# Kernel tuning notes

Measured on AMD Instinct MI355X. Metric: run time of the kernel, lower is better.

Reference implementation:

```python
import jax, jax.numpy as jnp
import numpy as np

N = 16384          # num nodes
E = 262144         # num edges (before self loops)
IN_DIM = 128
HID = 128
OUT = 2
TRIM = 0.1
MAX_DEG = 48       # padded max in-degree (incl. self loop); safe bound for Poisson(16)+1
BN_EPS = 1e-5


def _lin_params(key, fan_in, fan_out):
    kw, kb = jax.random.split(key)
    s = 1.0 / np.sqrt(fan_in)
    W = jax.random.uniform(kw, (fan_in, fan_out), jnp.float32, -s, s)
    b = jax.random.uniform(kb, (fan_out,), jnp.float32, -s, s)
    return W, b


def setup_inputs() -> dict:
    key = jax.random.key(0)
    ks = jax.random.split(key, 8)
    x = jax.random.normal(ks[0], (N, IN_DIM), jnp.float32)
    edge_index = jax.random.randint(ks[1], (2, E), 0, N, jnp.int32)
    Wl0, bl0 = _lin_params(ks[2], IN_DIM, HID)
    Wr0, br0 = _lin_params(ks[3], IN_DIM, HID)
    Wl1, bl1 = _lin_params(ks[4], HID, HID)
    Wr1, br1 = _lin_params(ks[5], HID, HID)
    Wl2, bl2 = _lin_params(ks[6], HID, OUT)
    Wr2, br2 = _lin_params(ks[7], HID, OUT)
    g0 = jnp.ones((HID,), jnp.float32); be0 = jnp.zeros((HID,), jnp.float32)
    g1 = jnp.ones((HID,), jnp.float32); be1 = jnp.zeros((HID,), jnp.float32)
    return dict(x=x, edge_index=edge_index,
                Wl0=Wl0, bl0=bl0, Wr0=Wr0, br0=br0, g0=g0, be0=be0,
                Wl1=Wl1, bl1=bl1, Wr1=Wr1, br1=br1, g1=g1, be1=be1,
                Wl2=Wl2, bl2=bl2, Wr2=Wr2, br2=br2)


def _forward(edge_index, x, Wl0, bl0, Wr0, br0, g0, be0,
             Wl1, bl1, Wr1, br1, g1, be1, Wl2, bl2, Wr2, br2):
    loops = jnp.arange(N, dtype=edge_index.dtype)
    row = jnp.concatenate([edge_index[0], loops])   # source nodes
    col = jnp.concatenate([edge_index[1], loops])   # destination nodes
    counts = jax.ops.segment_sum(jnp.ones_like(col), col, num_segments=N)  # in-degree, int
    deg = jnp.maximum(counts, 1).astype(x.dtype)
    norm = 1.0 / deg[col]                            # 1/deg(dst), per edge

    # Edge ordering grouped by destination node; rank = slot within the node's group.
    perm = jnp.argsort(col, stable=True)
    col_s = col[perm]
    starts = jnp.cumsum(counts) - counts
    rank = jnp.arange(col.shape[0], dtype=counts.dtype) - starts[col_s]
    node_id = jnp.where(rank < MAX_DEG, col_s, N)    # overflow slots -> OOB, dropped by scatter

    t = jnp.maximum(1, jnp.floor(counts.astype(jnp.float32) * TRIM).astype(counts.dtype))
    tcnt = counts - 2 * t
    pos = jnp.arange(MAX_DEG)[None, :]
    sel = (pos >= t[:, None]) & (pos < (counts - t)[:, None])   # [N, MAX_DEG]
    use_trim = (counts >= 5) & (tcnt > 0)
    inv_tcnt = 1.0 / jnp.maximum(tcnt, 1).astype(x.dtype)

    def trimmed_scatter(msg):
        # plain mean fallback
        mean = jax.ops.segment_sum(msg, col, num_segments=N) / deg[:, None]
        d = msg.shape[1]
        # padded per-node buffer; +inf pads sort to the end (never selected by `sel`)
        dense = jnp.full((N, MAX_DEG, d), jnp.inf, msg.dtype)
        dense = dense.at[node_id, rank].set(msg[perm], mode='drop')
        sdense = jnp.sort(dense, axis=1)             # per-feature sort within each node
        tmean = jnp.sum(jnp.where(sel[:, :, None], sdense, 0.0), axis=1) * inv_tcnt[:, None]
        return jnp.where(use_trim[:, None], tmean, mean)

    def conv(h, Wl, bl, Wr, br):
        msg = (h @ Wl + bl)[row] * norm[:, None]
        return trimmed_scatter(msg) + h @ Wr + br

    bn_scale = jnp.float32(1.0 / np.sqrt(1.0 + BN_EPS))  # eval-mode BN: running mean 0, var 1
    h = conv(x, Wl0, bl0, Wr0, br0)
    h = jax.nn.relu(h * bn_scale * g0 + be0)
    h = conv(h, Wl1, bl1, Wr1, br1)
    h = jax.nn.relu(h * bn_scale * g1 + be1)
    return conv(h, Wl2, bl2, Wr2, br2)


def reference(x, edge_index, Wl0, bl0, Wr0, br0, g0, be0,
              Wl1, bl1, Wr1, br1, g1, be1, Wl2, bl2, Wr2, br2):
    return _forward(edge_index, x, Wl0, bl0, Wr0, br0, g0, be0,
                    Wl1, bl1, Wr1, br1, g1, be1, Wl2, bl2, Wr2, br2)
```

## Files before the change

kernel.cpp:

```cpp
#include <hip/hip_runtime.h>
#include <hip/hip_bf16.h>
#include <hip/hip_fp16.h>
#include <math.h>

#define GN    16384
#define MAXD  48
#define BN_SCALE 0.9999950000374998f

typedef __attribute__((ext_vector_type(8))) short short8;
typedef __attribute__((ext_vector_type(4))) float f32x4;
typedef _Float16 __attribute__((ext_vector_type(2))) h2v;

__device__ inline short f2bf(float x) {
    unsigned u = __float_as_uint(x);
    return (short)((u + 0x7fffu + ((u >> 16) & 1u)) >> 16);
}
__device__ inline float bf2f(short s) {
    return __uint_as_float(((unsigned)(unsigned short)s) << 16);
}

__global__ __launch_bounds__(256) void k_build(
    const int* __restrict__ src, const int* __restrict__ dst, int E,
    int* __restrict__ adj, int* __restrict__ fill,
    const float* __restrict__ Wl0, const float* __restrict__ Wr0,
    const float* __restrict__ Wl1, const float* __restrict__ Wr1,
    short* __restrict__ W5)
{
    int idx = blockIdx.x * 256 + threadIdx.x;
    if (idx < E) {
        int dv = dst[idx];
        int slot = atomicAdd(&fill[dv], 1);
        if (slot < MAXD) adj[dv * MAXD + slot] = src[idx];
        return;
    }
    idx -= E;
    if (idx < GN) {
        int slot = atomicAdd(&fill[idx], 1);
        if (slot < MAXD) adj[idx * MAXD + slot] = idx;
        return;
    }
    idx -= GN;
    if (idx >= 2 * 8192) return;
    int layer = idx >> 13;
    int g     = idx & 8191;
    int split = (g >> 12) & 1;
    int ks    = (g >> 10) & 3;
    int nt    = (g >> 6) & 15;
    int l     = g & 63;
    int q = l >> 4, r = l & 15;
    int n = nt * 16 + r;
    const float* W = (n < 128) ? (layer ? Wl1 : Wl0) : (layer ? Wr1 : Wr0);
    int ncol = n & 127;
    short8 out;
    #pragma unroll
    for (int j = 0; j < 8; ++j) {
        int k = ks * 32 + (j >> 2) * 16 + q * 4 + (j & 3);
        float wv = W[k * 128 + ncol];
        short hi = f2bf(wv);
        out[j] = split ? f2bf(wv - bf2f(hi)) : hi;
    }
    *reinterpret_cast<short8*>(W5 + ((size_t)layer * 8192 + g) * 8) = out;
}

__global__ __launch_bounds__(256, 2) void k_gemm(
    const float* __restrict__ X, const short* __restrict__ W5,
    const float* __restrict__ bl, const float* __restrict__ br,
    _Float16* __restrict__ HL, float* __restrict__ HR)
{
    const int tid = threadIdx.x;
    const int w = tid >> 6, l = tid & 63;
    const int q = l >> 4, r = l & 15;
    const int half = w & 1, nhalf = w >> 1;
    const int rowA = blockIdx.x * 32 + half * 16 + r;

    short8 Ahi[4], Alo[4];
    const float4* xp = reinterpret_cast<const float4*>(X + (size_t)rowA * 128);
    #pragma unroll
    for (int h = 0; h < 8; ++h) {
        float4 v = xp[h * 4 + q];
        float xv[4] = {v.x, v.y, v.z, v.w};
        int ks = h >> 1, hk = h & 1;
        #pragma unroll
        for (int j = 0; j < 4; ++j) {
            short hi = f2bf(xv[j]);
            Ahi[ks][hk * 4 + j] = hi;
            Alo[ks][hk * 4 + j] = f2bf(xv[j] - bf2f(hi));
        }
    }

    const float* bias = nhalf ? br : bl;
    f32x4 acc[8];
    #pragma unroll
    for (int nt = 0; nt < 8; ++nt) {
        float b = bias[nt * 16 + r];
        acc[nt] = (f32x4){b, b, b, b};
    }

    #pragma unroll
    for (int ks = 0; ks < 4; ++ks) {
        #pragma unroll
        for (int nt = 0; nt < 8; ++nt) {
            int ntg = nhalf * 8 + nt;
            short8 Bhi = *reinterpret_cast<const short8*>(
                W5 + ((size_t)((ks) * 16 + ntg) * 64 + l) * 8);
            short8 Blo = *reinterpret_cast<const short8*>(
                W5 + ((size_t)((4 + ks) * 16 + ntg) * 64 + l) * 8);
            acc[nt] = __builtin_amdgcn_mfma_f32_16x16x32_bf16(Ahi[ks], Bhi, acc[nt], 0, 0, 0);
            acc[nt] = __builtin_amdgcn_mfma_f32_16x16x32_bf16(Ahi[ks], Blo, acc[nt], 0, 0, 0);
            acc[nt] = __builtin_amdgcn_mfma_f32_16x16x32_bf16(Alo[ks], Bhi, acc[nt], 0, 0, 0);
        }
    }

    const int rb = blockIdx.x * 32 + half * 16 + 4 * q;
    if (nhalf == 0) {
        #pragma unroll
        for (int nt = 0; nt < 8; ++nt) {
            int c = nt * 16 + r;
            #pragma unroll
            for (int j = 0; j < 4; ++j)
                HL[(size_t)(rb + j) * 128 + c] = (_Float16)acc[nt][j];
        }
    } else {
        #pragma unroll
        for (int nt = 0; nt < 8; ++nt) {
            int c = nt * 16 + r;
            #pragma unroll
            for (int j = 0; j < 4; ++j)
                HR[(size_t)(rb + j) * 128 + c] = acc[nt][j];
        }
    }
}

struct F2 { float x, y; };
__device__ inline F2 f2min(F2 a, F2 b) { return {fminf(a.x, b.x), fminf(a.y, b.y)}; }
__device__ inline F2 f2max(F2 a, F2 b) { return {fmaxf(a.x, b.x), fmaxf(a.y, b.y)}; }

__global__ __launch_bounds__(256) void k_agg(
    const _Float16* __restrict__ HL, const float* __restrict__ HR,
    const int* __restrict__ adj, const int* __restrict__ fill,
    const float* __restrict__ g, const float* __restrict__ be,
    float* __restrict__ hb)
{
    __shared__ int sadj[4][MAXD];
    const int tid = threadIdx.x, w = tid >> 6, l = tid & 63;
    const int v = blockIdx.x * 4 + w;
    const int cnt = fill[v];
    const int d = min(cnt, MAXD);
    if (l < d) sadj[w][l] = adj[v * MAXD + l] * 128;
    __syncthreads();

    const int f2i = l * 2;
    F2 tot = {0.f, 0.f};
    F2 s0 = { INFINITY,  INFINITY}, s1 = s0, s2 = s0, s3 = s0;
    F2 l0 = {-INFINITY, -INFINITY}, l1 = l0, l2 = l0, l3 = l0;

    if (cnt < 20) {
        for (int i = 0; i < d; ++i) {
            h2v hv = *reinterpret_cast<const h2v*>(HL + sadj[w][i] + f2i);
            F2 x = {(float)hv[0], (float)hv[1]};
            tot.x += x.x; tot.y += x.y;
            s0 = f2min(s0, x);
            l0 = f2max(l0, x);
        }
    } else {
        for (int i = 0; i < d; ++i) {
            h2v hv = *reinterpret_cast<const h2v*>(HL + sadj[w][i] + f2i);
            F2 x = {(float)hv[0], (float)hv[1]};
            tot.x += x.x; tot.y += x.y;
            F2 a = x;
            F2 t0 = f2min(s0, a); a = f2max(s0, a); s0 = t0;
            F2 t1 = f2min(s1, a); a = f2max(s1, a); s1 = t1;
            F2 t2 = f2min(s2, a); a = f2max(s2, a); s2 = t2;
            s3 = f2min(s3, a);
            F2 b = x;
            F2 u0 = f2max(l0, b); b = f2min(l0, b); l0 = u0;
            F2 u1 = f2max(l1, b); b = f2min(l1, b); l1 = u1;
            F2 u2 = f2max(l2, b); b = f2min(l2, b); l2 = u2;
            l3 = f2max(l3, b);
        }
    }

    int t = (int)floorf((float)cnt * 0.1f);
    if (t < 1) t = 1;
    int tcnt = cnt - 2 * t;
    bool use_trim = (cnt >= 5) && (tcnt > 0);
    float dd = (float)cnt;
    F2 res;
    if (use_trim) {
        int tt = min(t, 4);
        F2 bot = s0, top = l0;
        if (tt > 1) { bot.x += s1.x; bot.y += s1.y; top.x += l1.x; top.y += l1.y; }
        if (tt > 2) { bot.x += s2.x; bot.y += s2.y; top.x += l2.x; top.y += l2.y; }
        if (tt > 3) { bot.x += s3.x; bot.y += s3.y; top.x += l3.x; top.y += l3.y; }
        float inv = 1.0f / (dd * (float)tcnt);
        res.x = (tot.x - bot.x - top.x) * inv;
        res.y = (tot.y - bot.y - top.y) * inv;
    } else {
        float inv = 1.0f / (dd * dd);
        res.x = tot.x * inv;
        res.y = tot.y * inv;
    }

    const float2 hrv = *reinterpret_cast<const float2*>(HR + (size_t)v * 128 + f2i);
    float v0 = fmaxf((res.x + hrv.x) * (BN_SCALE * g[f2i])     + be[f2i],     0.f);
    float v1 = fmaxf((res.y + hrv.y) * (BN_SCALE * g[f2i + 1]) + be[f2i + 1], 0.f);
    float2 o = {v0, v1};
    *reinterpret_cast<float2*>(hb + (size_t)v * 128 + f2i) = o;
}

__global__ __launch_bounds__(256) void k_gemm_out(
    const float* __restrict__ H,
    const float* __restrict__ Wl, const float* __restrict__ bl,
    const float* __restrict__ Wr, const float* __restrict__ br,
    float* __restrict__ hl2, float* __restrict__ hr2)
{
    int idx = blockIdx.x * 256 + threadIdx.x;
    int v = idx >> 1, j = idx & 1;
    const float4* h = reinterpret_cast<const float4*>(H + (size_t)v * 128);
    float a = 0.f, rr = 0.f;
    #pragma unroll
    for (int k4 = 0; k4 < 32; ++k4) {
        float4 hv = h[k4];
        float xs[4] = {hv.x, hv.y, hv.z, hv.w};
        #pragma unroll
        for (int c = 0; c < 4; ++c) {
            int k = 4 * k4 + c;
            a  = fmaf(xs[c], Wl[k * 2 + j], a);
            rr = fmaf(xs[c], Wr[k * 2 + j], rr);
        }
    }
    hl2[idx] = a + bl[j];
    hr2[idx] = rr + br[j];
}

__global__ __launch_bounds__(256) void k_agg_out(
    const float* __restrict__ hl2, const float* __restrict__ hr2,
    const int* __restrict__ adj, const int* __restrict__ fill,
    float* __restrict__ out)
{
    int idx = blockIdx.x * 256 + threadIdx.x;
    int v = idx >> 1, j = idx & 1;
    int cnt = fill[v];
    int d = min(cnt, MAXD);
    const int* ap = adj + v * MAXD;

    float total = 0.f;
    float s0 = INFINITY, s1 = INFINITY, s2 = INFINITY, s3 = INFINITY;
    float l0 = -INFINITY, l1 = -INFINITY, l2 = -INFINITY, l3 = -INFINITY;
    for (int i = 0; i < d; ++i) {
        float x = hl2[ap[i] * 2 + j];
        total += x;
        float a = x;
        float t0 = fminf(s0, a); a = fmaxf(s0, a); s0 = t0;
        float t1 = fminf(s1, a); a = fmaxf(s1, a); s1 = t1;
        float t2 = fminf(s2, a); a = fmaxf(s2, a); s2 = t2;
        s3 = fminf(s3, a);
        float b = x;
        float u0 = fmaxf(l0, b); b = fminf(l0, b); l0 = u0;
        float u1 = fmaxf(l1, b); b = fminf(l1, b); l1 = u1;
        float u2 = fmaxf(l2, b); b = fminf(l2, b); l2 = u2;
        l3 = fmaxf(l3, b);
    }

    int t = (int)floorf((float)cnt * 0.1f);
    if (t < 1) t = 1;
    int tcnt = cnt - 2 * t;
    bool use_trim = (cnt >= 5) && (tcnt > 0);
    float dd = (float)cnt;
    float res;
    if (use_trim) {
        int tt = min(t, 4);
        float bot = s0, top = l0;
        if (tt > 1) { bot += s1; top += l1; }
        if (tt > 2) { bot += s2; top += l2; }
        if (tt > 3) { bot += s3; top += l3; }
        res = (total - bot - top) / (dd * (float)tcnt);
    } else {
        res = total / (dd * dd);
    }
    out[idx] = res + hr2[idx];
}

extern "C" void kernel_launch(void* const* d_in, const int* in_sizes, int n_in,
                              void* d_out, int out_size, void* d_ws, size_t ws_size,
                              hipStream_t stream)
{
    const float* x   = (const float*)d_in[0];
    const int*   ei  = (const int*)d_in[1];
    const int    E   = in_sizes[1] / 2;
    const float* Wl0 = (const float*)d_in[2];
    const float* bl0 = (const float*)d_in[3];
    const float* Wr0 = (const float*)d_in[4];
    const float* br0 = (const float*)d_in[5];
    const float* g0  = (const float*)d_in[6];
    const float* be0 = (const float*)d_in[7];
    const float* Wl1 = (const float*)d_in[8];
    const float* bl1 = (const float*)d_in[9];
    const float* Wr1 = (const float*)d_in[10];
    const float* br1 = (const float*)d_in[11];
    const float* g1  = (const float*)d_in[12];
    const float* be1 = (const float*)d_in[13];
    const float* Wl2 = (const float*)d_in[14];
    const float* bl2 = (const float*)d_in[15];
    const float* Wr2 = (const float*)d_in[16];
    const float* br2 = (const float*)d_in[17];
    float* out = (float*)d_out;

    char* w = (char*)d_ws;
    int*      adj  = (int*)w;       w += (size_t)GN * MAXD * 4;
    int*      fill = (int*)w;       w += (size_t)GN * 4;
    _Float16* HL   = (_Float16*)w;  w += (size_t)GN * 128 * 2;
    float*    HR   = (float*)w;     w += (size_t)GN * 128 * 4;
    float*    hb   = (float*)w;     w += (size_t)GN * 128 * 4;
    short*    W5   = (short*)w;     w += (size_t)2 * 8192 * 16;
    float*    hl2  = (float*)w;     w += (size_t)GN * 2 * 4;
    float*    hr2  = (float*)w;     w += (size_t)GN * 2 * 4;

    hipMemsetAsync(fill, 0, (size_t)GN * 4, stream);
    {
        int total = E + GN + 2 * 8192;
        k_build<<<(total + 255) / 256, 256, 0, stream>>>(
            ei, ei + E, E, adj, fill, Wl0, Wr0, Wl1, Wr1, W5);
    }

    k_gemm<<<GN / 32, 256, 0, stream>>>(x, W5, bl0, br0, HL, HR);
    k_agg <<<GN / 4, 256, 0, stream>>>(HL, HR, adj, fill, g0, be0, hb);
    k_gemm<<<GN / 32, 256, 0, stream>>>(hb, W5 + (size_t)8192 * 8, bl1, br1, HL, HR);
    k_agg <<<GN / 4, 256, 0, stream>>>(HL, HR, adj, fill, g1, be1, hb);
    k_gemm_out<<<GN * 2 / 256, 256, 0, stream>>>(hb, Wl2, bl2, Wr2, br2, hl2, hr2);
    k_agg_out <<<GN * 2 / 256, 256, 0, stream>>>(hl2, hr2, adj, fill, out);
}
```

Before: 200.2 us.

## Fuse all GNN stages into one cooperative persistent megakernel with grid syncs

Replaces the memset plus six separate kernel launches with a single cooperative kernel that runs each stage as a grid-stride phase separated by grid.sync(). The memset is folded in by having each node's fill counter start at 1 with its self loop in slot 0. Edge insertion into the adjacency lists now shares a phase with the first GEMM, so the two overlap. This removes launch gaps and inter-kernel drains, but the grid is capped at 512 blocks of 256 threads (2 per CU), which limits occupancy in the gather-heavy aggregation phases and adds grid-wide barrier cost.

```diff
diff --git a/kernel.cpp b/kernel.cpp
--- a/kernel.cpp
+++ b/kernel.cpp
@@ -1,7 +1,9 @@
 #include <hip/hip_runtime.h>
-#include <hip/hip_bf16.h>
+#include <hip/hip_cooperative_groups.h>
 #include <hip/hip_fp16.h>
 #include <math.h>
+
+namespace cg = cooperative_groups;
 
 #define GN    16384
 #define MAXD  48
@@ -19,114 +21,83 @@
     return __uint_as_float(((unsigned)(unsigned short)s) << 16);
 }
 
-__global__ __launch_bounds__(256) void k_build(
-    const int* __restrict__ src, const int* __restrict__ dst, int E,
-    int* __restrict__ adj, int* __restrict__ fill,
-    const float* __restrict__ Wl0, const float* __restrict__ Wr0,
-    const float* __restrict__ Wl1, const float* __restrict__ Wr1,
-    short* __restrict__ W5)
-{
-    int idx = blockIdx.x * 256 + threadIdx.x;
-    if (idx < E) {
-        int dv = dst[idx];
-        int slot = atomicAdd(&fill[dv], 1);
-        if (slot < MAXD) adj[dv * MAXD + slot] = src[idx];
-        return;
-    }
-    idx -= E;
-    if (idx < GN) {
-        int slot = atomicAdd(&fill[idx], 1);
-        if (slot < MAXD) adj[idx * MAXD + slot] = idx;
-        return;
-    }
-    idx -= GN;
-    if (idx >= 2 * 8192) return;
-    int layer = idx >> 13;
-    int g     = idx & 8191;
-    int split = (g >> 12) & 1;
-    int ks    = (g >> 10) & 3;
-    int nt    = (g >> 6) & 15;
-    int l     = g & 63;
-    int q = l >> 4, r = l & 15;
-    int n = nt * 16 + r;
-    const float* W = (n < 128) ? (layer ? Wl1 : Wl0) : (layer ? Wr1 : Wr0);
-    int ncol = n & 127;
-    short8 out;
-    #pragma unroll
-    for (int j = 0; j < 8; ++j) {
-        int k = ks * 32 + (j >> 2) * 16 + q * 4 + (j & 3);
-        float wv = W[k * 128 + ncol];
-        short hi = f2bf(wv);
-        out[j] = split ? f2bf(wv - bf2f(hi)) : hi;
-    }
-    *reinterpret_cast<short8*>(W5 + ((size_t)layer * 8192 + g) * 8) = out;
-}
-
-__global__ __launch_bounds__(256, 2) void k_gemm(
-    const float* __restrict__ X, const short* __restrict__ W5,
-    const float* __restrict__ bl, const float* __restrict__ br,
-    _Float16* __restrict__ HL, float* __restrict__ HR)
+struct Params {
+    const float* x; const int* ei; int E;
+    const float *Wl0, *bl0, *Wr0, *br0, *g0, *be0;
+    const float *Wl1, *bl1, *Wr1, *br1, *g1, *be1;
+    const float *Wl2, *bl2, *Wr2, *br2;
+    float* out;
+    int* adj; int* fill;
+    _Float16* HL; float* HR; float* hb;
+    short* W5; float* hl2; float* hr2;
+};
+
+__device__ inline void gemm_phase(const float* __restrict__ X,
+                                  const short* __restrict__ W5,
+                                  const float* __restrict__ bl,
+                                  const float* __restrict__ br,
+                                  _Float16* __restrict__ HL,
+                                  float* __restrict__ HR)
 {
     const int tid = threadIdx.x;
     const int w = tid >> 6, l = tid & 63;
     const int q = l >> 4, r = l & 15;
     const int half = w & 1, nhalf = w >> 1;
-    const int rowA = blockIdx.x * 32 + half * 16 + r;
-
-    short8 Ahi[4], Alo[4];
-    const float4* xp = reinterpret_cast<const float4*>(X + (size_t)rowA * 128);
-    #pragma unroll
-    for (int h = 0; h < 8; ++h) {
-        float4 v = xp[h * 4 + q];
-        float xv[4] = {v.x, v.y, v.z, v.w};
-        int ks = h >> 1, hk = h & 1;
-        #pragma unroll
-        for (int j = 0; j < 4; ++j) {
-            short hi = f2bf(xv[j]);
-            Ahi[ks][hk * 4 + j] = hi;
-            Alo[ks][hk * 4 + j] = f2bf(xv[j] - bf2f(hi));
-        }
-    }
-
-    const float* bias = nhalf ? br : bl;
-    f32x4 acc[8];
-    #pragma unroll
-    for (int nt = 0; nt < 8; ++nt) {
-        float b = bias[nt * 16 + r];
-        acc[nt] = (f32x4){b, b, b, b};
-    }
-
-    #pragma unroll
-    for (int ks = 0; ks < 4; ++ks) {
+
+    for (int tile = blockIdx.x; tile < GN / 32; tile += gridDim.x) {
+        const int rowA = tile * 32 + half * 16 + r;
+        short8 Ahi[4], Alo[4];
+        const float4* xp = reinterpret_cast<const float4*>(X + (size_t)rowA * 128);
+        #pragma unroll
+        for (int h = 0; h < 8; ++h) {
+            float4 v = xp[h * 4 + q];
+            float xv[4] = {v.x, v.y, v.z, v.w};
+            int ks = h >> 1, hk = h & 1;
+            #pragma unroll
+            for (int j = 0; j < 4; ++j) {
+                short hi = f2bf(xv[j]);
+                Ahi[ks][hk * 4 + j] = hi;
+                Alo[ks][hk * 4 + j] = f2bf(xv[j] - bf2f(hi));
+            }
+        }
+        const float* bias = nhalf ? br : bl;
+        f32x4 acc[8];
         #pragma unroll
         for (int nt = 0; nt < 8; ++nt) {
-            int ntg = nhalf * 8 + nt;
-            short8 Bhi = *reinterpret_cast<const short8*>(
-                W5 + ((size_t)((ks) * 16 + ntg) * 64 + l) * 8);
-            short8 Blo = *reinterpret_cast<const short8*>(
-                W5 + ((size_t)((4 + ks) * 16 + ntg) * 64 + l) * 8);
-            acc[nt] = __builtin_amdgcn_mfma_f32_16x16x32_bf16(Ahi[ks], Bhi, acc[nt], 0, 0, 0);
-            acc[nt] = __builtin_amdgcn_mfma_f32_16x16x32_bf16(Ahi[ks], Blo, acc[nt], 0, 0, 0);
-            acc[nt] = __builtin_amdgcn_mfma_f32_16x16x32_bf16(Alo[ks], Bhi, acc[nt], 0, 0, 0);
-        }
-    }
-
-    const int rb = blockIdx.x * 32 + half * 16 + 4 * q;
-    if (nhalf == 0) {
-        #pragma unroll
-        for (int nt = 0; nt < 8; ++nt) {
-            int c = nt * 16 + r;
-            #pragma unroll
-            for (int j = 0; j < 4; ++j)
-                HL[(size_t)(rb + j) * 128 + c] = (_Float16)acc[nt][j];
-        }
-    } else {
-        #pragma unroll
-        for (int nt = 0; nt < 8; ++nt) {
-            int c = nt * 16 + r;
-            #pragma unroll
-            for (int j = 0; j < 4; ++j)
-                HR[(size_t)(rb + j) * 128 + c] = acc[nt][j];
+            float b = bias[nt * 16 + r];
+            acc[nt] = (f32x4){b, b, b, b};
+        }
+        #pragma unroll
+        for (int ks = 0; ks < 4; ++ks) {
+            #pragma unroll
+            for (int nt = 0; nt < 8; ++nt) {
+                int ntg = nhalf * 8 + nt;
+                short8 Bhi = *reinterpret_cast<const short8*>(
+                    W5 + ((size_t)(ks * 16 + ntg) * 64 + l) * 8);
+                short8 Blo = *reinterpret_cast<const short8*>(
+                    W5 + ((size_t)((4 + ks) * 16 + ntg) * 64 + l) * 8);
+                acc[nt] = __builtin_amdgcn_mfma_f32_16x16x32_bf16(Ahi[ks], Bhi, acc[nt], 0, 0, 0);
+                acc[nt] = __builtin_amdgcn_mfma_f32_16x16x32_bf16(Ahi[ks], Blo, acc[nt], 0, 0, 0);
+                acc[nt] = __builtin_amdgcn_mfma_f32_16x16x32_bf16(Alo[ks], Bhi, acc[nt], 0, 0, 0);
+            }
+        }
+        const int rb = tile * 32 + half * 16 + 4 * q;
+        if (nhalf == 0) {
+            #pragma unroll
+            for (int nt = 0; nt < 8; ++nt) {
+                int c = nt * 16 + r;
+                #pragma unroll
+                for (int j = 0; j < 4; ++j)
+                    HL[(size_t)(rb + j) * 128 + c] = (_Float16)acc[nt][j];
+            }
+        } else {
+            #pragma unroll
+            for (int nt = 0; nt < 8; ++nt) {
+                int c = nt * 16 + r;
+                #pragma unroll
+                for (int j = 0; j < 4; ++j)
+                    HR[(size_t)(rb + j) * 128 + c] = acc[nt][j];
+            }
         }
     }
 }
@@ -135,198 +106,238 @@
 __device__ inline F2 f2min(F2 a, F2 b) { return {fminf(a.x, b.x), fminf(a.y, b.y)}; }
 __device__ inline F2 f2max(F2 a, F2 b) { return {fmaxf(a.x, b.x), fmaxf(a.y, b.y)}; }
 
-__global__ __launch_bounds__(256) void k_agg(
-    const _Float16* __restrict__ HL, const float* __restrict__ HR,
-    const int* __restrict__ adj, const int* __restrict__ fill,
-    const float* __restrict__ g, const float* __restrict__ be,
-    float* __restrict__ hb)
+__device__ inline void agg_phase(const _Float16* __restrict__ HL,
+                                 const float* __restrict__ HR,
+                                 const int* __restrict__ adj,
+                                 const int* __restrict__ fill,
+                                 const float* __restrict__ g,
+                                 const float* __restrict__ be,
+                                 float* __restrict__ hb,
+                                 int sadj[4][MAXD])
 {
+    const int tid = threadIdx.x, w = tid >> 6, l = tid & 63;
+    const int f2i = l * 2;
+    for (int gq = blockIdx.x; gq < GN / 4; gq += gridDim.x) {
+        const int v = gq * 4 + w;
+        const int cnt = fill[v];
+        const int d = min(cnt, MAXD);
+        if (l < d) sadj[w][l] = adj[v * MAXD + l] * 128;
+
+        F2 tot = {0.f, 0.f};
+        F2 s0 = { INFINITY,  INFINITY}, s1 = s0, s2 = s0, s3 = s0;
+        F2 l0 = {-INFINITY, -INFINITY}, l1 = l0, l2 = l0, l3 = l0;
+
+        if (cnt < 20) {
+            for (int i = 0; i < d; ++i) {
+                h2v hv = *reinterpret_cast<const h2v*>(HL + sadj[w][i] + f2i);
+                F2 x = {(float)hv[0], (float)hv[1]};
+                tot.x += x.x; tot.y += x.y;
+                s0 = f2min(s0, x);
+                l0 = f2max(l0, x);
+            }
+        } else {
+            for (int i = 0; i < d; ++i) {
+                h2v hv = *reinterpret_cast<const h2v*>(HL + sadj[w][i] + f2i);
+                F2 x = {(float)hv[0], (float)hv[1]};
+                tot.x += x.x; tot.y += x.y;
+                F2 a = x;
+                F2 t0 = f2min(s0, a); a = f2max(s0, a); s0 = t0;
+                F2 t1 = f2min(s1, a); a = f2max(s1, a); s1 = t1;
+                F2 t2 = f2min(s2, a); a = f2max(s2, a); s2 = t2;
+                s3 = f2min(s3, a);
+                F2 b = x;
+                F2 u0 = f2max(l0, b); b = f2min(l0, b); l0 = u0;
+                F2 u1 = f2max(l1, b); b = f2min(l1, b); l1 = u1;
+                F2 u2 = f2max(l2, b); b = f2min(l2, b); l2 = u2;
+                l3 = f2max(l3, b);
+            }
+        }
+
+        int t = (int)floorf((float)cnt * 0.1f);
+        if (t < 1) t = 1;
+        int tcnt = cnt - 2 * t;
+        bool use_trim = (cnt >= 5) && (tcnt > 0);
+        float dd = (float)cnt;
+        F2 res;
+        if (use_trim) {
+            int tt = min(t, 4);
+            F2 bot = s0, top = l0;
+            if (tt > 1) { bot.x += s1.x; bot.y += s1.y; top.x += l1.x; top.y += l1.y; }
+            if (tt > 2) { bot.x += s2.x; bot.y += s2.y; top.x += l2.x; top.y += l2.y; }
+            if (tt > 3) { bot.x += s3.x; bot.y += s3.y; top.x += l3.x; top.y += l3.y; }
+            float inv = 1.0f / (dd * (float)tcnt);
+            res.x = (tot.x - bot.x - top.x) * inv;
+            res.y = (tot.y - bot.y - top.y) * inv;
+        } else {
+            float inv = 1.0f / (dd * dd);
+            res.x = tot.x * inv;
+            res.y = tot.y * inv;
+        }
+
+        const float2 hrv = *reinterpret_cast<const float2*>(HR + (size_t)v * 128 + f2i);
+        float v0 = fmaxf((res.x + hrv.x) * (BN_SCALE * g[f2i])     + be[f2i],     0.f);
+        float v1 = fmaxf((res.y + hrv.y) * (BN_SCALE * g[f2i + 1]) + be[f2i + 1], 0.f);
+        float2 o = {v0, v1};
+        *reinterpret_cast<float2*>(hb + (size_t)v * 128 + f2i) = o;
+    }
+}
+
+__global__ __launch_bounds__(256, 2) void k_mega(Params p)
+{
+    cg::grid_group grid = cg::this_grid();
     __shared__ int sadj[4][MAXD];
-    const int tid = threadIdx.x, w = tid >> 6, l = tid & 63;
-    const int v = blockIdx.x * 4 + w;
-    const int cnt = fill[v];
-    const int d = min(cnt, MAXD);
-    if (l < d) sadj[w][l] = adj[v * MAXD + l] * 128;
-    __syncthreads();
-
-    const int f2i = l * 2;
-    F2 tot = {0.f, 0.f};
-    F2 s0 = { INFINITY,  INFINITY}, s1 = s0, s2 = s0, s3 = s0;
-    F2 l0 = {-INFINITY, -INFINITY}, l1 = l0, l2 = l0, l3 = l0;
-
-    if (cnt < 20) {
+    const int tid  = threadIdx.x;
+    const int nthr = gridDim.x * 256;
+    const int gtid = blockIdx.x * 256 + tid;
+
+    for (int v = gtid; v < GN; v += nthr) {
+        p.fill[v] = 1;
+        p.adj[v * MAXD] = v;
+    }
+    for (int t = gtid; t < 2 * 8192; t += nthr) {
+        int layer = t >> 13;
+        int g     = t & 8191;
+        int split = (g >> 12) & 1;
+        int ks    = (g >> 10) & 3;
+        int nt    = (g >> 6) & 15;
+        int l     = g & 63;
+        int q = l >> 4, r = l & 15;
+        int n = nt * 16 + r;
+        const float* W = (n < 128) ? (layer ? p.Wl1 : p.Wl0)
+                                   : (layer ? p.Wr1 : p.Wr0);
+        int ncol = n & 127;
+        short8 o8;
+        #pragma unroll
+        for (int j = 0; j < 8; ++j) {
+            int k = ks * 32 + (j >> 2) * 16 + q * 4 + (j & 3);
+            float wv = W[k * 128 + ncol];
+            short hi = f2bf(wv);
+            o8[j] = split ? f2bf(wv - bf2f(hi)) : hi;
+        }
+        *reinterpret_cast<short8*>(p.W5 + ((size_t)layer * 8192 + g) * 8) = o8;
+    }
+    grid.sync();
+
+    {
+        const int* src = p.ei;
+        const int* dst = p.ei + p.E;
+        for (int e = gtid; e < p.E; e += nthr) {
+            int dv = dst[e];
+            int slot = atomicAdd(&p.fill[dv], 1);
+            if (slot < MAXD) p.adj[dv * MAXD + slot] = src[e];
+        }
+    }
+    gemm_phase(p.x, p.W5, p.bl0, p.br0, p.HL, p.HR);
+    grid.sync();
+
+    agg_phase(p.HL, p.HR, p.adj, p.fill, p.g0, p.be0, p.hb, sadj);
+    grid.sync();
+
+    gemm_phase(p.hb, p.W5 + (size_t)8192 * 8, p.bl1, p.br1, p.HL, p.HR);
+    grid.sync();
+
+    agg_phase(p.HL, p.HR, p.adj, p.fill, p.g1, p.be1, p.hb, sadj);
+    grid.sync();
+
+    for (int idx = gtid; idx < 2 * GN; idx += nthr) {
+        int v = idx >> 1, j = idx & 1;
+        const float4* h = reinterpret_cast<const float4*>(p.hb + (size_t)v * 128);
+        float a = 0.f, rr = 0.f;
+        #pragma unroll
+        for (int k4 = 0; k4 < 32; ++k4) {
+            float4 hv = h[k4];
+            float xs[4] = {hv.x, hv.y, hv.z, hv.w};
+            #pragma unroll
+            for (int c = 0; c < 4; ++c) {
+                int k = 4 * k4 + c;
+                a  = fmaf(xs[c], p.Wl2[k * 2 + j], a);
+                rr = fmaf(xs[c], p.Wr2[k * 2 + j], rr);
+            }
+        }
+        p.hl2[idx] = a + p.bl2[j];
+        p.hr2[idx] = rr + p.br2[j];
+    }
+    grid.sync();
+
+    for (int idx = gtid; idx < 2 * GN; idx += nthr) {
+        int v = idx >> 1, j = idx & 1;
+        int cnt = p.fill[v];
+        int d = min(cnt, MAXD);
+        const int* ap = p.adj + v * MAXD;
+
+        float total = 0.f;
+        float s0 = INFINITY, s1 = INFINITY, s2 = INFINITY, s3 = INFINITY;
+        float l0 = -INFINITY, l1 = -INFINITY, l2 = -INFINITY, l3 = -INFINITY;
         for (int i = 0; i < d; ++i) {
-            h2v hv = *reinterpret_cast<const h2v*>(HL + sadj[w][i] + f2i);
-            F2 x = {(float)hv[0], (float)hv[1]};
-            tot.x += x.x; tot.y += x.y;
-            s0 = f2min(s0, x);
-            l0 = f2max(l0, x);
-        }
-    } else {
-        for (int i = 0; i < d; ++i) {
-            h2v hv = *reinterpret_cast<const h2v*>(HL + sadj[w][i] + f2i);
-            F2 x = {(float)hv[0], (float)hv[1]};
-            tot.x += x.x; tot.y += x.y;
-            F2 a = x;
-            F2 t0 = f2min(s0, a); a = f2max(s0, a); s0 = t0;
-            F2 t1 = f2min(s1, a); a = f2max(s1, a); s1 = t1;
-            F2 t2 = f2min(s2, a); a = f2max(s2, a); s2 = t2;
-            s3 = f2min(s3, a);
-            F2 b = x;
-            F2 u0 = f2max(l0, b); b = f2min(l0, b); l0 = u0;
-            F2 u1 = f2max(l1, b); b = f2min(l1, b); l1 = u1;
-            F2 u2 = f2max(l2, b); b = f2min(l2, b); l2 = u2;
-            l3 = f2max(l3, b);
-        }
-    }
-
-    int t = (int)floorf((float)cnt * 0.1f);
-    if (t < 1) t = 1;
-    int tcnt = cnt - 2 * t;
-    bool use_trim = (cnt >= 5) && (tcnt > 0);
-    float dd = (float)cnt;
-    F2 res;
-    if (use_trim) {
-        int tt = min(t, 4);
-        F2 bot = s0, top = l0;
-        if (tt > 1) { bot.x += s1.x; bot.y += s1.y; top.x += l1.x; top.y += l1.y; }
-        if (tt > 2) { bot.x += s2.x; bot.y += s2.y; top.x += l2.x; top.y += l2.y; }
-        if (tt > 3) { bot.x += s3.x; bot.y += s3.y; top.x += l3.x; top.y += l3.y; }
-        float inv = 1.0f / (dd * (float)tcnt);
-        res.x = (tot.x - bot.x - top.x) * inv;
-        res.y = (tot.y - bot.y - top.y) * inv;
-    } else {
-        float inv = 1.0f / (dd * dd);
-        res.x = tot.x * inv;
-        res.y = tot.y * inv;
-    }
-
-    const float2 hrv = *reinterpret_cast<const float2*>(HR + (size_t)v * 128 + f2i);
-    float v0 = fmaxf((res.x + hrv.x) * (BN_SCALE * g[f2i])     + be[f2i],     0.f);
-    float v1 = fmaxf((res.y + hrv.y) * (BN_SCALE * g[f2i + 1]) + be[f2i + 1], 0.f);
-    float2 o = {v0, v1};
-    *reinterpret_cast<float2*>(hb + (size_t)v * 128 + f2i) = o;
-}
-
-__global__ __launch_bounds__(256) void k_gemm_out(
-    const float* __restrict__ H,
-    const float* __restrict__ Wl, const float* __restrict__ bl,
-    const float* __restrict__ Wr, const float* __restrict__ br,
-    float* __restrict__ hl2, float* __restrict__ hr2)
-{
-    int idx = blockIdx.x * 256 + threadIdx.x;
-    int v = idx >> 1, j = idx & 1;
-    const float4* h = reinterpret_cast<const float4*>(H + (size_t)v * 128);
-    float a = 0.f, rr = 0.f;
-    #pragma unroll
-    for (int k4 = 0; k4 < 32; ++k4) {
-        float4 hv = h[k4];
-        float xs[4] = {hv.x, hv.y, hv.z, hv.w};
-        #pragma unroll
-        for (int c = 0; c < 4; ++c) {
-            int k = 4 * k4 + c;
-            a  = fmaf(xs[c], Wl[k * 2 + j], a);
-            rr = fmaf(xs[c], Wr[k * 2 + j], rr);
-        }
-    }
-    hl2[idx] = a + bl[j];
-    hr2[idx] = rr + br[j];
-}
-
-__global__ __launch_bounds__(256) void k_agg_out(
-    const float* __restrict__ hl2, const float* __restrict__ hr2,
-    const int* __restrict__ adj, const int* __restrict__ fill,
-    float* __restrict__ out)
-{
-    int idx = blockIdx.x * 256 + threadIdx.x;
-    int v = idx >> 1, j = idx & 1;
-    int cnt = fill[v];
-    int d = min(cnt, MAXD);
-    const int* ap = adj + v * MAXD;
-
-    float total = 0.f;
-    float s0 = INFINITY, s1 = INFINITY, s2 = INFINITY, s3 = INFINITY;
-    float l0 = -INFINITY, l1 = -INFINITY, l2 = -INFINITY, l3 = -INFINITY;
-    for (int i = 0; i < d; ++i) {
-        float x = hl2[ap[i] * 2 + j];
-        total += x;
-        float a = x;
-        float t0 = fminf(s0, a); a = fmaxf(s0, a); s0 = t0;
-        float t1 = fminf(s1, a); a = fmaxf(s1, a); s1 = t1;
-        float t2 = fminf(s2, a); a = fmaxf(s2, a); s2 = t2;
-        s3 = fminf(s3, a);
-        float b = x;
-        float u0 = fmaxf(l0, b); b = fminf(l0, b); l0 = u0;
-        float u1 = fmaxf(l1, b); b = fminf(l1, b); l1 = u1;
-        float u2 = fmaxf(l2, b); b = fminf(l2, b); l2 = u2;
-        l3 = fmaxf(l3, b);
-    }
-
-    int t = (int)floorf((float)cnt * 0.1f);
-    if (t < 1) t = 1;
-    int tcnt = cnt - 2 * t;
-    bool use_trim = (cnt >= 5) && (tcnt > 0);
-    float dd = (float)cnt;
-    float res;
-    if (use_trim) {
-        int tt = min(t, 4);
-        float bot = s0, top = l0;
-        if (tt > 1) { bot += s1; top += l1; }
-        if (tt > 2) { bot += s2; top += l2; }
-        if (tt > 3) { bot += s3; top += l3; }
-        res = (total - bot - top) / (dd * (float)tcnt);
-    } else {
-        res = total / (dd * dd);
-    }
-    out[idx] = res + hr2[idx];
+            float xv = p.hl2[ap[i] * 2 + j];
+            total += xv;
+            float a = xv;
+            float t0 = fminf(s0, a); a = fmaxf(s0, a); s0 = t0;
+            float t1 = fminf(s1, a); a = fmaxf(s1, a); s1 = t1;
+            float t2 = fminf(s2, a); a = fmaxf(s2, a); s2 = t2;
+            s3 = fminf(s3, a);
+            float b = xv;
+            float u0 = fmaxf(l0, b); b = fminf(l0, b); l0 = u0;
+            float u1 = fmaxf(l1, b); b = fminf(l1, b); l1 = u1;
+            float u2 = fmaxf(l2, b); b = fminf(l2, b); l2 = u2;
+            l3 = fmaxf(l3, b);
+        }
+
+        int t = (int)floorf((float)cnt * 0.1f);
+        if (t < 1) t = 1;
+        int tcnt = cnt - 2 * t;
+        bool use_trim = (cnt >= 5) && (tcnt > 0);
+        float dd = (float)cnt;
+        float res;
+        if (use_trim) {
+            int tt = min(t, 4);
+            float bot = s0, top = l0;
+            if (tt > 1) { bot += s1; top += l1; }
+            if (tt > 2) { bot += s2; top += l2; }
+            if (tt > 3) { bot += s3; top += l3; }
+            res = (total - bot - top) / (dd * (float)tcnt);
+        } else {
+            res = total / (dd * dd);
+        }
+        p.out[idx] = res + p.hr2[idx];
+    }
 }
 
 extern "C" void kernel_launch(void* const* d_in, const int* in_sizes, int n_in,
                               void* d_out, int out_size, void* d_ws, size_t ws_size,
                               hipStream_t stream)
 {
-    const float* x   = (const float*)d_in[0];
-    const int*   ei  = (const int*)d_in[1];
-    const int    E   = in_sizes[1] / 2;
-    const float* Wl0 = (const float*)d_in[2];
-    const float* bl0 = (const float*)d_in[3];
-    const float* Wr0 = (const float*)d_in[4];
-    const float* br0 = (const float*)d_in[5];
-    const float* g0  = (const float*)d_in[6];
-    const float* be0 = (const float*)d_in[7];
-    const float* Wl1 = (const float*)d_in[8];
-    const float* bl1 = (const float*)d_in[9];
-    const float* Wr1 = (const float*)d_in[10];
-    const float* br1 = (const float*)d_in[11];
-    const float* g1  = (const float*)d_in[12];
-    const float* be1 = (const float*)d_in[13];
-    const float* Wl2 = (const float*)d_in[14];
-    const float* bl2 = (const float*)d_in[15];
-    const float* Wr2 = (const float*)d_in[16];
-    const float* br2 = (const float*)d_in[17];
-    float* out = (float*)d_out;
+    Params p;
+    p.x   = (const float*)d_in[0];
+    p.ei  = (const int*)d_in[1];
+    p.E   = in_sizes[1] / 2;
+    p.Wl0 = (const float*)d_in[2];  p.bl0 = (const float*)d_in[3];
+    p.Wr0 = (const float*)d_in[4];  p.br0 = (const float*)d_in[5];
+    p.g0  = (const float*)d_in[6];  p.be0 = (const float*)d_in[7];
+    p.Wl1 = (const float*)d_in[8];  p.bl1 = (const float*)d_in[9];
+    p.Wr1 = (const float*)d_in[10]; p.br1 = (const float*)d_in[11];
+    p.g1  = (const float*)d_in[12]; p.be1 = (const float*)d_in[13];
+    p.Wl2 = (const float*)d_in[14]; p.bl2 = (const float*)d_in[15];
+    p.Wr2 = (const float*)d_in[16]; p.br2 = (const float*)d_in[17];
+    p.out = (float*)d_out;
 
     char* w = (char*)d_ws;
-    int*      adj  = (int*)w;       w += (size_t)GN * MAXD * 4;
-    int*      fill = (int*)w;       w += (size_t)GN * 4;
-    _Float16* HL   = (_Float16*)w;  w += (size_t)GN * 128 * 2;
-    float*    HR   = (float*)w;     w += (size_t)GN * 128 * 4;
-    float*    hb   = (float*)w;     w += (size_t)GN * 128 * 4;
-    short*    W5   = (short*)w;     w += (size_t)2 * 8192 * 16;
-    float*    hl2  = (float*)w;     w += (size_t)GN * 2 * 4;
-    float*    hr2  = (float*)w;     w += (size_t)GN * 2 * 4;
-
-    hipMemsetAsync(fill, 0, (size_t)GN * 4, stream);
-    {
-        int total = E + GN + 2 * 8192;
-        k_build<<<(total + 255) / 256, 256, 0, stream>>>(
-            ei, ei + E, E, adj, fill, Wl0, Wr0, Wl1, Wr1, W5);
-    }
-
-    k_gemm<<<GN / 32, 256, 0, stream>>>(x, W5, bl0, br0, HL, HR);
-    k_agg <<<GN / 4, 256, 0, stream>>>(HL, HR, adj, fill, g0, be0, hb);
-    k_gemm<<<GN / 32, 256, 0, stream>>>(hb, W5 + (size_t)8192 * 8, bl1, br1, HL, HR);
-    k_agg <<<GN / 4, 256, 0, stream>>>(HL, HR, adj, fill, g1, be1, hb);
-    k_gemm_out<<<GN * 2 / 256, 256, 0, stream>>>(hb, Wl2, bl2, Wr2, br2, hl2, hr2);
-    k_agg_out <<<GN * 2 / 256, 256, 0, stream>>>(hl2, hr2, adj, fill, out);
-}
+    p.adj  = (int*)w;       w += (size_t)GN * MAXD * 4;
+    p.fill = (int*)w;       w += (size_t)GN * 4;
+    p.HL   = (_Float16*)w;  w += (size_t)GN * 128 * 2;
+    p.HR   = (float*)w;     w += (size_t)GN * 128 * 4;
+    p.hb   = (float*)w;     w += (size_t)GN * 128 * 4;
+    p.W5   = (short*)w;     w += (size_t)2 * 8192 * 16;
+    p.hl2  = (float*)w;     w += (size_t)GN * 2 * 4;
+    p.hr2  = (float*)w;     w += (size_t)GN * 2 * 4;
+
+    int nb = 0;
+    hipOccupancyMaxActiveBlocksPerMultiprocessor(&nb, k_mega, 256, 0);
+    if (nb < 1) nb = 1;
+    long long cap = (long long)nb * 256;
+    int grid = (int)(cap < 512 ? cap : 512);
+
+    void* args[] = {(void*)&p};
+    hipLaunchCooperativeKernel((const void*)k_mega, dim3(grid), dim3(256),
+                               args, 0, stream);
+}
```

Measured after the change: 511.1 us. +155.3%, slower.

## Fuse aggregation with next-layer GEMM and overlap adjacency build with first GEMM

Applied to the files above, without the earlier changes.

The adjacency build now runs in the same launch as the layer-0 GEMM, on extra blocks. The layer-0 aggregation is fused with the layer-1 GEMM through a shared-memory tile of 32 nodes. The layer-1 aggregation is fused with the tiny output projection using a wave shuffle reduction. The memset is folded into the weight-prep kernel. This removes the intermediate hb round trips and several launches, but each wave in the fused layer-1 kernel now processes 8 nodes serially, which lowers parallelism for the latency-bound gathers.

```diff
diff --git a/kernel.cpp b/kernel.cpp
--- a/kernel.cpp
+++ b/kernel.cpp
@@ -1,5 +1,4 @@
 #include <hip/hip_runtime.h>
-#include <hip/hip_bf16.h>
 #include <hip/hip_fp16.h>
 #include <math.h>
 
@@ -19,144 +18,20 @@
     return __uint_as_float(((unsigned)(unsigned short)s) << 16);
 }
 
-__global__ __launch_bounds__(256) void k_build(
-    const int* __restrict__ src, const int* __restrict__ dst, int E,
-    int* __restrict__ adj, int* __restrict__ fill,
-    const float* __restrict__ Wl0, const float* __restrict__ Wr0,
-    const float* __restrict__ Wl1, const float* __restrict__ Wr1,
-    short* __restrict__ W5)
-{
-    int idx = blockIdx.x * 256 + threadIdx.x;
-    if (idx < E) {
-        int dv = dst[idx];
-        int slot = atomicAdd(&fill[dv], 1);
-        if (slot < MAXD) adj[dv * MAXD + slot] = src[idx];
-        return;
-    }
-    idx -= E;
-    if (idx < GN) {
-        int slot = atomicAdd(&fill[idx], 1);
-        if (slot < MAXD) adj[idx * MAXD + slot] = idx;
-        return;
-    }
-    idx -= GN;
-    if (idx >= 2 * 8192) return;
-    int layer = idx >> 13;
-    int g     = idx & 8191;
-    int split = (g >> 12) & 1;
-    int ks    = (g >> 10) & 3;
-    int nt    = (g >> 6) & 15;
-    int l     = g & 63;
-    int q = l >> 4, r = l & 15;
-    int n = nt * 16 + r;
-    const float* W = (n < 128) ? (layer ? Wl1 : Wl0) : (layer ? Wr1 : Wr0);
-    int ncol = n & 127;
-    short8 out;
-    #pragma unroll
-    for (int j = 0; j < 8; ++j) {
-        int k = ks * 32 + (j >> 2) * 16 + q * 4 + (j & 3);
-        float wv = W[k * 128 + ncol];
-        short hi = f2bf(wv);
-        out[j] = split ? f2bf(wv - bf2f(hi)) : hi;
-    }
-    *reinterpret_cast<short8*>(W5 + ((size_t)layer * 8192 + g) * 8) = out;
-}
-
-__global__ __launch_bounds__(256, 2) void k_gemm(
-    const float* __restrict__ X, const short* __restrict__ W5,
-    const float* __restrict__ bl, const float* __restrict__ br,
-    _Float16* __restrict__ HL, float* __restrict__ HR)
-{
-    const int tid = threadIdx.x;
-    const int w = tid >> 6, l = tid & 63;
-    const int q = l >> 4, r = l & 15;
-    const int half = w & 1, nhalf = w >> 1;
-    const int rowA = blockIdx.x * 32 + half * 16 + r;
-
-    short8 Ahi[4], Alo[4];
-    const float4* xp = reinterpret_cast<const float4*>(X + (size_t)rowA * 128);
-    #pragma unroll
-    for (int h = 0; h < 8; ++h) {
-        float4 v = xp[h * 4 + q];
-        float xv[4] = {v.x, v.y, v.z, v.w};
-        int ks = h >> 1, hk = h & 1;
-        #pragma unroll
-        for (int j = 0; j < 4; ++j) {
-            short hi = f2bf(xv[j]);
-            Ahi[ks][hk * 4 + j] = hi;
-            Alo[ks][hk * 4 + j] = f2bf(xv[j] - bf2f(hi));
-        }
-    }
-
-    const float* bias = nhalf ? br : bl;
-    f32x4 acc[8];
-    #pragma unroll
-    for (int nt = 0; nt < 8; ++nt) {
-        float b = bias[nt * 16 + r];
-        acc[nt] = (f32x4){b, b, b, b};
-    }
-
-    #pragma unroll
-    for (int ks = 0; ks < 4; ++ks) {
-        #pragma unroll
-        for (int nt = 0; nt < 8; ++nt) {
-            int ntg = nhalf * 8 + nt;
-            short8 Bhi = *reinterpret_cast<const short8*>(
-                W5 + ((size_t)((ks) * 16 + ntg) * 64 + l) * 8);
-            short8 Blo = *reinterpret_cast<const short8*>(
-                W5 + ((size_t)((4 + ks) * 16 + ntg) * 64 + l) * 8);
-            acc[nt] = __builtin_amdgcn_mfma_f32_16x16x32_bf16(Ahi[ks], Bhi, acc[nt], 0, 0, 0);
-            acc[nt] = __builtin_amdgcn_mfma_f32_16x16x32_bf16(Ahi[ks], Blo, acc[nt], 0, 0, 0);
-            acc[nt] = __builtin_amdgcn_mfma_f32_16x16x32_bf16(Alo[ks], Bhi, acc[nt], 0, 0, 0);
-        }
-    }
-
-    const int rb = blockIdx.x * 32 + half * 16 + 4 * q;
-    if (nhalf == 0) {
-        #pragma unroll
-        for (int nt = 0; nt < 8; ++nt) {
-            int c = nt * 16 + r;
-            #pragma unroll
-            for (int j = 0; j < 4; ++j)
-                HL[(size_t)(rb + j) * 128 + c] = (_Float16)acc[nt][j];
-        }
-    } else {
-        #pragma unroll
-        for (int nt = 0; nt < 8; ++nt) {
-            int c = nt * 16 + r;
-            #pragma unroll
-            for (int j = 0; j < 4; ++j)
-                HR[(size_t)(rb + j) * 128 + c] = acc[nt][j];
-        }
-    }
-}
-
 struct F2 { float x, y; };
 __device__ inline F2 f2min(F2 a, F2 b) { return {fminf(a.x, b.x), fminf(a.y, b.y)}; }
 __device__ inline F2 f2max(F2 a, F2 b) { return {fmaxf(a.x, b.x), fmaxf(a.y, b.y)}; }
 
-__global__ __launch_bounds__(256) void k_agg(
-    const _Float16* __restrict__ HL, const float* __restrict__ HR,
-    const int* __restrict__ adj, const int* __restrict__ fill,
-    const float* __restrict__ g, const float* __restrict__ be,
-    float* __restrict__ hb)
-{
-    __shared__ int sadj[4][MAXD];
-    const int tid = threadIdx.x, w = tid >> 6, l = tid & 63;
-    const int v = blockIdx.x * 4 + w;
-    const int cnt = fill[v];
-    const int d = min(cnt, MAXD);
-    if (l < d) sadj[w][l] = adj[v * MAXD + l] * 128;
-    __syncthreads();
-
-    const int f2i = l * 2;
+__device__ inline F2 trim_core(const _Float16* __restrict__ HL,
+                               const int* __restrict__ srow, int cnt, int d, int f2i)
+{
     F2 tot = {0.f, 0.f};
     F2 s0 = { INFINITY,  INFINITY}, s1 = s0, s2 = s0, s3 = s0;
     F2 l0 = {-INFINITY, -INFINITY}, l1 = l0, l2 = l0, l3 = l0;
 
     if (cnt < 20) {
         for (int i = 0; i < d; ++i) {
-            h2v hv = *reinterpret_cast<const h2v*>(HL + sadj[w][i] + f2i);
+            h2v hv = *reinterpret_cast<const h2v*>(HL + srow[i] + f2i);
             F2 x = {(float)hv[0], (float)hv[1]};
             tot.x += x.x; tot.y += x.y;
             s0 = f2min(s0, x);
@@ -164,7 +39,7 @@
         }
     } else {
         for (int i = 0; i < d; ++i) {
-            h2v hv = *reinterpret_cast<const h2v*>(HL + sadj[w][i] + f2i);
+            h2v hv = *reinterpret_cast<const h2v*>(HL + srow[i] + f2i);
             F2 x = {(float)hv[0], (float)hv[1]};
             tot.x += x.x; tot.y += x.y;
             F2 a = x;
@@ -200,37 +75,214 @@
         res.x = tot.x * inv;
         res.y = tot.y * inv;
     }
-
-    const float2 hrv = *reinterpret_cast<const float2*>(HR + (size_t)v * 128 + f2i);
-    float v0 = fmaxf((res.x + hrv.x) * (BN_SCALE * g[f2i])     + be[f2i],     0.f);
-    float v1 = fmaxf((res.y + hrv.y) * (BN_SCALE * g[f2i + 1]) + be[f2i + 1], 0.f);
-    float2 o = {v0, v1};
-    *reinterpret_cast<float2*>(hb + (size_t)v * 128 + f2i) = o;
-}
-
-__global__ __launch_bounds__(256) void k_gemm_out(
-    const float* __restrict__ H,
-    const float* __restrict__ Wl, const float* __restrict__ bl,
-    const float* __restrict__ Wr, const float* __restrict__ br,
+    return res;
+}
+
+__global__ __launch_bounds__(256) void k_prep(
+    int* __restrict__ fill,
+    const float* __restrict__ Wl0, const float* __restrict__ Wr0,
+    const float* __restrict__ Wl1, const float* __restrict__ Wr1,
+    short* __restrict__ W5)
+{
+    int t = blockIdx.x * 256 + threadIdx.x;
+    fill[t] = 0;
+
+    int layer = t >> 13;
+    int g     = t & 8191;
+    int split = (g >> 12) & 1;
+    int ks    = (g >> 10) & 3;
+    int nt    = (g >> 6) & 15;
+    int l     = g & 63;
+    int q = l >> 4, r = l & 15;
+    int n = nt * 16 + r;
+    const float* W = (n < 128) ? (layer ? Wl1 : Wl0) : (layer ? Wr1 : Wr0);
+    int ncol = n & 127;
+    short8 o8;
+    #pragma unroll
+    for (int j = 0; j < 8; ++j) {
+        int k = ks * 32 + (j >> 2) * 16 + q * 4 + (j & 3);
+        float wv = W[k * 128 + ncol];
+        short hi = f2bf(wv);
+        o8[j] = split ? f2bf(wv - bf2f(hi)) : hi;
+    }
+    *reinterpret_cast<short8*>(W5 + ((size_t)layer * 8192 + g) * 8) = o8;
+}
+
+__device__ inline void gemm_tile(const short8 Ahi[4], const short8 Alo[4],
+                                 const short* __restrict__ W5,
+                                 const float* __restrict__ bl,
+                                 const float* __restrict__ br,
+                                 _Float16* __restrict__ HL, float* __restrict__ HR,
+                                 int tile, int half, int nhalf, int q, int r, int l)
+{
+    const float* bias = nhalf ? br : bl;
+    f32x4 acc[8];
+    #pragma unroll
+    for (int nt = 0; nt < 8; ++nt) {
+        float b = bias[nt * 16 + r];
+        acc[nt] = (f32x4){b, b, b, b};
+    }
+    #pragma unroll
+    for (int ks = 0; ks < 4; ++ks) {
+        #pragma unroll
+        for (int nt = 0; nt < 8; ++nt) {
+            int ntg = nhalf * 8 + nt;
+            short8 Bhi = *reinterpret_cast<const short8*>(
+                W5 + ((size_t)(ks * 16 + ntg) * 64 + l) * 8);
+            short8 Blo = *reinterpret_cast<const short8*>(
+                W5 + ((size_t)((4 + ks) * 16 + ntg) * 64 + l) * 8);
+            acc[nt] = __builtin_amdgcn_mfma_f32_16x16x32_bf16(Ahi[ks], Bhi, acc[nt], 0, 0, 0);
+            acc[nt] = __builtin_amdgcn_mfma_f32_16x16x32_bf16(Ahi[ks], Blo, acc[nt], 0, 0, 0);
+            acc[nt] = __builtin_amdgcn_mfma_f32_16x16x32_bf16(Alo[ks], Bhi, acc[nt], 0, 0, 0);
+        }
+    }
+    const int rb = tile * 32 + half * 16 + 4 * q;
+    if (nhalf == 0) {
+        #pragma unroll
+        for (int nt = 0; nt < 8; ++nt) {
+            int c = nt * 16 + r;
+            #pragma unroll
+            for (int j = 0; j < 4; ++j)
+                HL[(size_t)(rb + j) * 128 + c] = (_Float16)acc[nt][j];
+        }
+    } else {
+        #pragma unroll
+        for (int nt = 0; nt < 8; ++nt) {
+            int c = nt * 16 + r;
+            #pragma unroll
+            for (int j = 0; j < 4; ++j)
+                HR[(size_t)(rb + j) * 128 + c] = acc[nt][j];
+        }
+    }
+}
+
+__global__ __launch_bounds__(256) void k_fused0(
+    const float* __restrict__ X, const int* __restrict__ ei, int E,
+    int* __restrict__ adj, int* __restrict__ fill,
+    const short* __restrict__ W5,
+    const float* __restrict__ bl, const float* __restrict__ br,
+    _Float16* __restrict__ HL, float* __restrict__ HR)
+{
+    const int tid = threadIdx.x;
+    if (blockIdx.x >= 512) {
+        const int* src = ei;
+        const int* dst = ei + E;
+        int g0 = (blockIdx.x - 512) * 256 + tid;
+        for (int i = g0; i < E + GN; i += 128 * 256) {
+            int s, dv;
+            if (i < E) { s = src[i]; dv = dst[i]; }
+            else       { s = i - E;  dv = i - E; }
+            int slot = atomicAdd(&fill[dv], 1);
+            if (slot < MAXD) adj[dv * MAXD + slot] = s;
+        }
+        return;
+    }
+    const int w = tid >> 6, l = tid & 63;
+    const int q = l >> 4, r = l & 15;
+    const int half = w & 1, nhalf = w >> 1;
+    const int rowA = blockIdx.x * 32 + half * 16 + r;
+
+    short8 Ahi[4], Alo[4];
+    const float4* xp = reinterpret_cast<const float4*>(X + (size_t)rowA * 128);
+    #pragma unroll
+    for (int h = 0; h < 8; ++h) {
+        float4 v = xp[h * 4 + q];
+        float xv[4] = {v.x, v.y, v.z, v.w};
+        int ks = h >> 1, hk = h & 1;
+        #pragma unroll
+        for (int j = 0; j < 4; ++j) {
+            short hi = f2bf(xv[j]);
+            Ahi[ks][hk * 4 + j] = hi;
+            Alo[ks][hk * 4 + j] = f2bf(xv[j] - bf2f(hi));
+        }
+    }
+    gemm_tile(Ahi, Alo, W5, bl, br, HL, HR, blockIdx.x, half, nhalf, q, r, l);
+}
+
+__global__ __launch_bounds__(256) void k_fused1(
+    const _Float16* __restrict__ HL0, const float* __restrict__ HR0,
+    const int* __restrict__ adj, const int* __restrict__ fill,
+    const float* __restrict__ g, const float* __restrict__ be,
+    const short* __restrict__ W5,
+    const float* __restrict__ bl, const float* __restrict__ br,
+    _Float16* __restrict__ HL1, float* __restrict__ HR1)
+{
+    __shared__ float hbs[32][132];
+    __shared__ int sadj[4][MAXD];
+    const int tid = threadIdx.x, w = tid >> 6, l = tid & 63;
+    const int f2i = l * 2;
+    const int v0 = blockIdx.x * 32;
+
+    for (int s = 0; s < 8; ++s) {
+        const int v = v0 + w * 8 + s;
+        const int cnt = fill[v];
+        const int d = min(cnt, MAXD);
+        if (l < d) sadj[w][l] = adj[v * MAXD + l] * 128;
+        F2 res = trim_core(HL0, sadj[w], cnt, d, f2i);
+        const float2 hrv = *reinterpret_cast<const float2*>(HR0 + (size_t)v * 128 + f2i);
+        hbs[w * 8 + s][f2i]     = fmaxf((res.x + hrv.x) * (BN_SCALE * g[f2i])     + be[f2i],     0.f);
+        hbs[w * 8 + s][f2i + 1] = fmaxf((res.y + hrv.y) * (BN_SCALE * g[f2i + 1]) + be[f2i + 1], 0.f);
+    }
+    __syncthreads();
+
+    const int q = l >> 4, r = l & 15;
+    const int half = w & 1, nhalf = w >> 1;
+    const int m = half * 16 + r;
+    short8 Ahi[4], Alo[4];
+    #pragma unroll
+    for (int h = 0; h < 8; ++h) {
+        float4 vv = *reinterpret_cast<const float4*>(&hbs[m][h * 16 + 4 * q]);
+        float xv[4] = {vv.x, vv.y, vv.z, vv.w};
+        int ks = h >> 1, hk = h & 1;
+        #pragma unroll
+        for (int j = 0; j < 4; ++j) {
+            short hi = f2bf(xv[j]);
+            Ahi[ks][hk * 4 + j] = hi;
+            Alo[ks][hk * 4 + j] = f2bf(xv[j] - bf2f(hi));
+        }
+    }
+    gemm_tile(Ahi, Alo, W5, bl, br, HL1, HR1, blockIdx.x, half, nhalf, q, r, l);
+}
+
+__global__ __launch_bounds__(256) void k_fused2(
+    const _Float16* __restrict__ HL1, const float* __restrict__ HR1,
+    const int* __restrict__ adj, const int* __restrict__ fill,
+    const float* __restrict__ g, const float* __restrict__ be,
+    const float* __restrict__ Wl2, const float* __restrict__ bl2,
+    const float* __restrict__ Wr2, const float* __restrict__ br2,
     float* __restrict__ hl2, float* __restrict__ hr2)
 {
-    int idx = blockIdx.x * 256 + threadIdx.x;
-    int v = idx >> 1, j = idx & 1;
-    const float4* h = reinterpret_cast<const float4*>(H + (size_t)v * 128);
-    float a = 0.f, rr = 0.f;
-    #pragma unroll
-    for (int k4 = 0; k4 < 32; ++k4) {
-        float4 hv = h[k4];
-        float xs[4] = {hv.x, hv.y, hv.z, hv.w};
-        #pragma unroll
-        for (int c = 0; c < 4; ++c) {
-            int k = 4 * k4 + c;
-            a  = fmaf(xs[c], Wl[k * 2 + j], a);
-            rr = fmaf(xs[c], Wr[k * 2 + j], rr);
-        }
-    }
-    hl2[idx] = a + bl[j];
-    hr2[idx] = rr + br[j];
+    __shared__ int sadj[4][MAXD];
+    const int tid = threadIdx.x, w = tid >> 6, l = tid & 63;
+    const int f2i = l * 2;
+    const int v = blockIdx.x * 4 + w;
+    const int cnt = fill[v];
+    const int d = min(cnt, MAXD);
+    if (l < d) sadj[w][l] = adj[v * MAXD + l] * 128;
+    F2 res = trim_core(HL1, sadj[w], cnt, d, f2i);
+    const float2 hrv = *reinterpret_cast<const float2*>(HR1 + (size_t)v * 128 + f2i);
+    float h0 = fmaxf((res.x + hrv.x) * (BN_SCALE * g[f2i])     + be[f2i],     0.f);
+    float h1 = fmaxf((res.y + hrv.y) * (BN_SCALE * g[f2i + 1]) + be[f2i + 1], 0.f);
+
+    float4 wl = *reinterpret_cast<const float4*>(Wl2 + l * 4);
+    float4 wr = *reinterpret_cast<const float4*>(Wr2 + l * 4);
+    float p0 = h0 * wl.x + h1 * wl.z;
+    float p1 = h0 * wl.y + h1 * wl.w;
+    float p2 = h0 * wr.x + h1 * wr.z;
+    float p3 = h0 * wr.y + h1 * wr.w;
+    #pragma unroll
+    for (int off = 1; off < 64; off <<= 1) {
+        p0 += __shfl_xor(p0, off);
+        p1 += __shfl_xor(p1, off);
+        p2 += __shfl_xor(p2, off);
+        p3 += __shfl_xor(p3, off);
+    }
+    if (l == 0) {
+        hl2[v * 2 + 0] = p0 + bl2[0];
+        hl2[v * 2 + 1] = p1 + bl2[1];
+        hr2[v * 2 + 0] = p2 + br2[0];
+        hr2[v * 2 + 1] = p3 + br2[1];
+    }
 }
 
 __global__ __launch_bounds__(256) void k_agg_out(
@@ -309,24 +361,19 @@
     char* w = (char*)d_ws;
     int*      adj  = (int*)w;       w += (size_t)GN * MAXD * 4;
     int*      fill = (int*)w;       w += (size_t)GN * 4;
-    _Float16* HL   = (_Float16*)w;  w += (size_t)GN * 128 * 2;
-    float*    HR   = (float*)w;     w += (size_t)GN * 128 * 4;
-    float*    hb   = (float*)w;     w += (size_t)GN * 128 * 4;
+    _Float16* HL0  = (_Float16*)w;  w += (size_t)GN * 128 * 2;
+    float*    HR0  = (float*)w;     w += (size_t)GN * 128 * 4;
+    _Float16* HL1  = (_Float16*)w;  w += (size_t)GN * 128 * 2;
+    float*    HR1  = (float*)w;     w += (size_t)GN * 128 * 4;
     short*    W5   = (short*)w;     w += (size_t)2 * 8192 * 16;
     float*    hl2  = (float*)w;     w += (size_t)GN * 2 * 4;
     float*    hr2  = (float*)w;     w += (size_t)GN * 2 * 4;
 
-    hipMemsetAsync(fill, 0, (size_t)GN * 4, stream);
-    {
-        int total = E + GN + 2 * 8192;
-        k_build<<<(total + 255) / 256, 256, 0, stream>>>(
-            ei, ei + E, E, adj, fill, Wl0, Wr0, Wl1, Wr1, W5);
-    }
-
-    k_gemm<<<GN / 32, 256, 0, stream>>>(x, W5, bl0, br0, HL, HR);
-    k_agg <<<GN / 4, 256, 0, stream>>>(HL, HR, adj, fill, g0, be0, hb);
-    k_gemm<<<GN / 32, 256, 0, stream>>>(hb, W5 + (size_t)8192 * 8, bl1, br1, HL, HR);
-    k_agg <<<GN / 4, 256, 0, stream>>>(HL, HR, adj, fill, g1, be1, hb);
-    k_gemm_out<<<GN * 2 / 256, 256, 0, stream>>>(hb, Wl2, bl2, Wr2, br2, hl2, hr2);
-    k_agg_out <<<GN * 2 / 256, 256, 0, stream>>>(hl2, hr2, adj, fill, out);
-}
+    k_prep  <<<GN / 256, 256, 0, stream>>>(fill, Wl0, Wr0, Wl1, Wr1, W5);
+    k_fused0<<<640, 256, 0, stream>>>(x, ei, E, adj, fill, W5, bl0, br0, HL0, HR0);
+    k_fused1<<<GN / 32, 256, 0, stream>>>(HL0, HR0, adj, fill, g0, be0,
+                                          W5 + (size_t)8192 * 8, bl1, br1, HL1, HR1);
+    k_fused2<<<GN / 4, 256, 0, stream>>>(HL1, HR1, adj, fill, g1, be1,
+                                         Wl2, bl2, Wr2, br2, hl2, hr2);
+    k_agg_out<<<GN * 2 / 256, 256, 0, stream>>>(hl2, hr2, adj, fill, out);
+}
```

Result: faster. 194.9 us (-2.6%).
